# Kernel tuning notes

Measured on AMD Instinct MI355X. Metric: run time of the kernel, lower is better.

The kernel has to match this reference:

```python
import jax, jax.numpy as jnp
import numpy as np

F_TOT = 108
OUT_CH = 5
GNN_IN = 5


def setup_inputs() -> dict:
    key = jax.random.key(0)
    ks = jax.random.split(key, 24)
    B, S, N, E = 16, 1, 20000, 320000
    s = 0.1  # param init scale
    d = {}
    d["x"] = jax.random.normal(ks[0], (B, S, N, F_TOT), jnp.float32)
    d["edge_index"] = jax.random.randint(ks[1], (2, E), 0, N, dtype=jnp.int32)
    # four Conv1d(1, 5, k=24) branches
    for i, nm in enumerate(["t", "r", "tp", "ssr"]):
        d[f"w_{nm}"] = s * jax.random.normal(ks[2 + 2 * i], (OUT_CH, 1, 24), jnp.float32)
        d[f"b_{nm}"] = s * jax.random.normal(ks[3 + 2 * i], (OUT_CH,), jnp.float32)
    # fc1: 32 -> 20, fc2: 20 -> 5
    d["fc1_w"] = s * jax.random.normal(ks[10], (20, 12 + 4 * OUT_CH), jnp.float32)
    d["fc1_b"] = s * jax.random.normal(ks[11], (20,), jnp.float32)
    d["fc2_w"] = s * jax.random.normal(ks[12], (GNN_IN, 20), jnp.float32)
    d["fc2_b"] = s * jax.random.normal(ks[13], (GNN_IN,), jnp.float32)
    # SAGEConv(5 -> 20): lin_l (with bias, applied to mean-aggregated neighbors), lin_r (no bias, root)
    d["g1_wl"] = s * jax.random.normal(ks[14], (20, GNN_IN), jnp.float32)
    d["g1_bl"] = s * jax.random.normal(ks[15], (20,), jnp.float32)
    d["g1_wr"] = s * jax.random.normal(ks[16], (20, GNN_IN), jnp.float32)
    # SAGEConv(20 -> 1)
    d["g2_wl"] = s * jax.random.normal(ks[17], (1, 20), jnp.float32)
    d["g2_bl"] = s * jax.random.normal(ks[18], (1,), jnp.float32)
    d["g2_wr"] = s * jax.random.normal(ks[19], (1, 20), jnp.float32)
    return d


def _branch(xs, w, b):
    # Conv1d(in=1, out=5, k=24) over a length-24 window == a single dot product per channel.
    # xs: [NB, 24], w: [5, 1, 24] -> [NB, 5], then ReLU
    return jax.nn.relu(jnp.einsum('nk,ok->no', xs, w[:, 0, :]) + b)


def _sage(h, src, dst, wl, bl, wr, n_nodes):
    # PyG SAGEConv with mean aggregation: out = lin_l(mean_{j in N(i)} x_j) + lin_r(x_i)
    # h: [B, N, d]
    msg = jnp.transpose(h[:, src, :], (1, 0, 2))                    # [E, B, d]
    agg = jax.ops.segment_sum(msg, dst, num_segments=n_nodes)       # [N, B, d]
    deg = jax.ops.segment_sum(jnp.ones((src.shape[0],), h.dtype), dst, num_segments=n_nodes)
    mean = jnp.transpose(agg, (1, 0, 2)) / jnp.maximum(deg, 1.0)[None, :, None]  # [B, N, d]
    return mean @ wl.T + bl + h @ wr.T


def reference(x, edge_index, w_t, b_t, w_r, b_r, w_tp, b_tp, w_ssr, b_ssr,
              fc1_w, fc1_b, fc2_w, fc2_b, g1_wl, g1_bl, g1_wr, g2_wl, g2_bl, g2_wr):
    B, S, N, F = x.shape
    src, dst = edge_index[0], edge_index[1]
    # permute(2,0,1,3).reshape(N*B, S, F); S == 1
    xs = jnp.transpose(x, (2, 0, 1, 3)).reshape(N * B, S, F)[:, 0, :]  # [NB, 108]
    out_t = _branch(xs[:, 12:36], w_t, b_t)
    out_r = _branch(xs[:, 36:60], w_r, b_r)
    out_tp = _branch(xs[:, 60:84], w_tp, b_tp)
    out_ssr = _branch(xs[:, 84:108], w_ssr, b_ssr)
    feat = jnp.concatenate([xs[:, :12], out_t, out_r, out_tp, out_ssr], axis=1)  # [NB, 32]
    h = jax.nn.relu(feat @ fc1_w.T + fc1_b) @ fc2_w.T + fc2_b                    # [NB, 5]
    h = jnp.transpose(h.reshape(N, B, -1), (1, 0, 2))                            # [B, N, 5]
    h = _sage(h, src, dst, g1_wl, g1_bl, g1_wr, N)                               # [B, N, 20]
    h = _sage(h, src, dst, g2_wl, g2_bl, g2_wr, N)                               # [B, N, 1]
    return jnp.transpose(h, (0, 2, 1))                                           # [B, 1, N]
```

## Files before the change

### kernel.cpp

```cpp
#include <hip/hip_runtime.h>


__global__ void k_coefs(const float* __restrict__ g1_wl, const float* __restrict__ g1_bl,
                        const float* __restrict__ g1_wr, const float* __restrict__ g2_wl,
                        const float* __restrict__ g2_wr, float* __restrict__ coef) {
  if (blockIdx.x == 0 && threadIdx.x == 0) {
    for (int k = 0; k < 5; ++k) {
      float a = 0.f, r1 = 0.f, c = 0.f, r2 = 0.f;
      for (int j = 0; j < 20; ++j) {
        float wl = g1_wl[j * 5 + k], wr = g1_wr[j * 5 + k];
        a  += g2_wl[j] * wl;
        r1 += g2_wr[j] * wl;
        c  += g2_wl[j] * wr;
        r2 += g2_wr[j] * wr;
      }
      coef[k] = a; coef[5 + k] = r1; coef[10 + k] = c; coef[15 + k] = r2;
    }
    float kb1 = 0.f, kb2 = 0.f;
    for (int j = 0; j < 20; ++j) { kb1 += g2_wl[j] * g1_bl[j]; kb2 += g2_wr[j] * g1_bl[j]; }
    coef[20] = kb1; coef[21] = kb2;
  }
}

__global__ void k_deg(const int* __restrict__ dst, int E, int* __restrict__ degi) {
  int e = blockIdx.x * blockDim.x + threadIdx.x;
  if (e < E) atomicAdd(&degi[dst[e]], 1);
}

__global__ void k_inv(const int* __restrict__ degi, float* __restrict__ invd, int N) {
  int n = blockIdx.x * blockDim.x + threadIdx.x;
  if (n < N) invd[n] = 1.0f / fmaxf((float)degi[n], 1.0f);
}

__global__ __launch_bounds__(256) void k_mlp(
    const float* __restrict__ x,
    const float* __restrict__ w_t, const float* __restrict__ b_t,
    const float* __restrict__ w_r, const float* __restrict__ b_r,
    const float* __restrict__ w_tp, const float* __restrict__ b_tp,
    const float* __restrict__ w_ssr, const float* __restrict__ b_ssr,
    const float* __restrict__ f1w, const float* __restrict__ f1b,
    const float* __restrict__ f2w, const float* __restrict__ f2b,
    const float* __restrict__ coef,
    float* __restrict__ F1, float* __restrict__ F2, int N, int rows) {
  int rr = blockIdx.x * 256 + threadIdx.x;
  if (rr >= rows) return;
  const float* xp = x + (size_t)rr * 108;

  float feat[32];
#pragma unroll
  for (int i = 0; i < 3; ++i) {
    float4 v = *reinterpret_cast<const float4*>(xp + 4 * i);
    feat[4 * i + 0] = v.x; feat[4 * i + 1] = v.y; feat[4 * i + 2] = v.z; feat[4 * i + 3] = v.w;
  }
  const float* cw[4] = {w_t, w_r, w_tp, w_ssr};
  const float* cb[4] = {b_t, b_r, b_tp, b_ssr};
#pragma unroll
  for (int br = 0; br < 4; ++br) {
    float win[24];
#pragma unroll
    for (int i = 0; i < 6; ++i) {
      float4 v = *reinterpret_cast<const float4*>(xp + 12 + br * 24 + 4 * i);
      win[4 * i + 0] = v.x; win[4 * i + 1] = v.y; win[4 * i + 2] = v.z; win[4 * i + 3] = v.w;
    }
#pragma unroll
    for (int o = 0; o < 5; ++o) {
      float acc = cb[br][o];
#pragma unroll
      for (int k = 0; k < 24; ++k) acc = fmaf(win[k], cw[br][o * 24 + k], acc);
      feat[12 + br * 5 + o] = fmaxf(acc, 0.f);
    }
  }
  float h20[20];
#pragma unroll
  for (int o = 0; o < 20; ++o) {
    float acc = f1b[o];
#pragma unroll
    for (int i = 0; i < 32; ++i) acc = fmaf(feat[i], f1w[o * 32 + i], acc);
    h20[o] = fmaxf(acc, 0.f);
  }
  float h5[5];
#pragma unroll
  for (int o = 0; o < 5; ++o) {
    float acc = f2b[o];
#pragma unroll
    for (int i = 0; i < 20; ++i) acc = fmaf(h20[i], f2w[o * 20 + i], acc);
    h5[o] = acc;
  }
  float sa = 0.f, sr1 = 0.f, sc = 0.f, sr2 = 0.f;
#pragma unroll
  for (int k = 0; k < 5; ++k) {
    sa  = fmaf(h5[k], coef[k],      sa);
    sr1 = fmaf(h5[k], coef[5 + k],  sr1);
    sc  = fmaf(h5[k], coef[10 + k], sc);
    sr2 = fmaf(h5[k], coef[15 + k], sr2);
  }
  int b = rr / N;
  int n = rr - b * N;
  reinterpret_cast<float2*>(F1)[n * 16 + b] = make_float2(sa, sr1);
  reinterpret_cast<float2*>(F2)[n * 16 + b] = make_float2(sc, sr2);
}

__global__ void k_agg1(const int* __restrict__ src, const int* __restrict__ dst, int E,
                       const float* __restrict__ F1, float* __restrict__ A1) {
  int t = blockIdx.x * blockDim.x + threadIdx.x;
  int e = t >> 5, j = t & 31;
  if (e < E) {
    int s = src[e], d = dst[e];
    atomicAdd(&A1[d * 32 + j], F1[s * 32 + j]);
  }
}

__global__ void k_fin1(const float* __restrict__ A1, const float* __restrict__ F2,
                       const float* __restrict__ invd, float* __restrict__ W, int N) {
  int t = blockIdx.x * blockDim.x + threadIdx.x;
  if (t < N * 16) {
    int n = t >> 4, b = t & 15;
    W[t] = A1[n * 32 + 2 * b] * invd[n] + F2[n * 32 + 2 * b];
  }
}

__global__ void k_agg2(const int* __restrict__ src, const int* __restrict__ dst, int E,
                       const float* __restrict__ W, float* __restrict__ A2) {
  int t = blockIdx.x * blockDim.x + threadIdx.x;
  int e = t >> 4, b = t & 15;
  if (e < E) {
    int s = src[e], d = dst[e];
    atomicAdd(&A2[d * 16 + b], W[s * 16 + b]);
  }
}

__global__ void k_final(const float* __restrict__ A1, const float* __restrict__ F2,
                        const float* __restrict__ A2, const float* __restrict__ invd,
                        const int* __restrict__ degi, const float* __restrict__ coef,
                        const float* __restrict__ g2_bl, float* __restrict__ out, int N) {
  int t = blockIdx.x * blockDim.x + threadIdx.x;
  if (t < 16 * N) {
    int b = t / N, n = t - b * N;
    float inv = invd[n];
    float chi = degi[n] > 0 ? 1.f : 0.f;
    float kb1 = coef[20], kb2 = coef[21], bl2 = g2_bl[0];
    out[t] = (A2[n * 16 + b] + A1[n * 32 + 2 * b + 1]) * inv
             + F2[n * 32 + 2 * b + 1] + kb1 * chi + kb2 + bl2;
  }
}

extern "C" void kernel_launch(void* const* d_in, const int* in_sizes, int n_in,
                              void* d_out, int out_size, void* d_ws, size_t ws_size,
                              hipStream_t stream) {
  const float* x     = (const float*)d_in[0];
  const int*   ei    = (const int*)d_in[1];
  const float* w_t   = (const float*)d_in[2];
  const float* b_t   = (const float*)d_in[3];
  const float* w_r   = (const float*)d_in[4];
  const float* b_r   = (const float*)d_in[5];
  const float* w_tp  = (const float*)d_in[6];
  const float* b_tp  = (const float*)d_in[7];
  const float* w_ssr = (const float*)d_in[8];
  const float* b_ssr = (const float*)d_in[9];
  const float* f1w   = (const float*)d_in[10];
  const float* f1b   = (const float*)d_in[11];
  const float* f2w   = (const float*)d_in[12];
  const float* f2b   = (const float*)d_in[13];
  const float* g1_wl = (const float*)d_in[14];
  const float* g1_bl = (const float*)d_in[15];
  const float* g1_wr = (const float*)d_in[16];
  const float* g2_wl = (const float*)d_in[17];
  const float* g2_bl = (const float*)d_in[18];
  const float* g2_wr = (const float*)d_in[19];
  float* out = (float*)d_out;

  const int E = in_sizes[1] / 2;
  const int N = out_size / 16;
  const int rows = out_size;
  const int* src = ei;
  const int* dst = ei + E;

  float* ws   = (float*)d_ws;
  float* coef = ws;
  int*   degi = (int*)(ws + 32);
  float* invd = ws + 32 + N;
  float* F1   = invd + N;
  float* F2   = F1 + (size_t)32 * N;
  float* A1   = F2 + (size_t)32 * N;
  float* A2   = A1 + (size_t)32 * N;
  float* W    = A2 + (size_t)16 * N;

  hipMemsetAsync(degi, 0, (size_t)N * sizeof(int), stream);
  hipMemsetAsync(A1, 0, (size_t)N * 32 * sizeof(float), stream);
  hipMemsetAsync(A2, 0, (size_t)N * 16 * sizeof(float), stream);

  k_coefs<<<1, 64, 0, stream>>>(g1_wl, g1_bl, g1_wr, g2_wl, g2_wr, coef);
  k_deg<<<(E + 255) / 256, 256, 0, stream>>>(dst, E, degi);
  k_inv<<<(N + 255) / 256, 256, 0, stream>>>(degi, invd, N);
  k_mlp<<<(rows + 255) / 256, 256, 0, stream>>>(
      x, w_t, b_t, w_r, b_r, w_tp, b_tp, w_ssr, b_ssr,
      f1w, f1b, f2w, f2b, coef, F1, F2, N, rows);
  {
    long long t1 = (long long)E * 32;
    k_agg1<<<(int)((t1 + 255) / 256), 256, 0, stream>>>(src, dst, E, F1, A1);
  }
  k_fin1<<<(N * 16 + 255) / 256, 256, 0, stream>>>(A1, F2, invd, W, N);
  {
    long long t2 = (long long)E * 16;
    k_agg2<<<(int)((t2 + 255) / 256), 256, 0, stream>>>(src, dst, E, W, A2);
  }
  k_final<<<(16 * N + 255) / 256, 256, 0, stream>>>(A1, F2, A2, invd, degi, coef, g2_bl, out, N);
}
```

Measured before the change: 149.6 us.

## Fuse memsets, degree count and coefficient precompute into existing kernels

Removes the three memsets and the coefficient, degree and inverse-degree kernels. Zeroing of the accumulators and degree array moves into the MLP kernel, and degree counting moves into the first aggregation, which now uses 16 threads per edge with float2 loads. Inverse degree and the SAGE coefficient contractions are recomputed inline in each thread, adding some arithmetic per thread. The MLP kernel also preloads the whole 108-float row into registers and reorders the conv loops. The aim is to cut kernel-launch count and extra passes over memory.

```diff
diff --git a/kernel.cpp b/kernel.cpp
--- a/kernel.cpp
+++ b/kernel.cpp
@@ -1,36 +1,5 @@
 #include <hip/hip_runtime.h>
 
-
-__global__ void k_coefs(const float* __restrict__ g1_wl, const float* __restrict__ g1_bl,
-                        const float* __restrict__ g1_wr, const float* __restrict__ g2_wl,
-                        const float* __restrict__ g2_wr, float* __restrict__ coef) {
-  if (blockIdx.x == 0 && threadIdx.x == 0) {
-    for (int k = 0; k < 5; ++k) {
-      float a = 0.f, r1 = 0.f, c = 0.f, r2 = 0.f;
-      for (int j = 0; j < 20; ++j) {
-        float wl = g1_wl[j * 5 + k], wr = g1_wr[j * 5 + k];
-        a  += g2_wl[j] * wl;
-        r1 += g2_wr[j] * wl;
-        c  += g2_wl[j] * wr;
-        r2 += g2_wr[j] * wr;
-      }
-      coef[k] = a; coef[5 + k] = r1; coef[10 + k] = c; coef[15 + k] = r2;
-    }
-    float kb1 = 0.f, kb2 = 0.f;
-    for (int j = 0; j < 20; ++j) { kb1 += g2_wl[j] * g1_bl[j]; kb2 += g2_wr[j] * g1_bl[j]; }
-    coef[20] = kb1; coef[21] = kb2;
-  }
-}
-
-__global__ void k_deg(const int* __restrict__ dst, int E, int* __restrict__ degi) {
-  int e = blockIdx.x * blockDim.x + threadIdx.x;
-  if (e < E) atomicAdd(&degi[dst[e]], 1);
-}
-
-__global__ void k_inv(const int* __restrict__ degi, float* __restrict__ invd, int N) {
-  int n = blockIdx.x * blockDim.x + threadIdx.x;
-  if (n < N) invd[n] = 1.0f / fmaxf((float)degi[n], 1.0f);
-}
 
 __global__ __launch_bounds__(256) void k_mlp(
     const float* __restrict__ x,
@@ -40,36 +9,47 @@
     const float* __restrict__ w_ssr, const float* __restrict__ b_ssr,
     const float* __restrict__ f1w, const float* __restrict__ f1b,
     const float* __restrict__ f2w, const float* __restrict__ f2b,
-    const float* __restrict__ coef,
-    float* __restrict__ F1, float* __restrict__ F2, int N, int rows) {
+    const float* __restrict__ g1_wl, const float* __restrict__ g1_wr,
+    const float* __restrict__ g2_wl, const float* __restrict__ g2_wr,
+    float* __restrict__ F1, float* __restrict__ F2,
+    int* __restrict__ degi, float* __restrict__ A1, float* __restrict__ A2,
+    int N, int rows) {
   int rr = blockIdx.x * 256 + threadIdx.x;
   if (rr >= rows) return;
-  const float* xp = x + (size_t)rr * 108;
+
+  const float4* xv = reinterpret_cast<const float4*>(x + (size_t)rr * 108);
+  float4 v[27];
+#pragma unroll
+  for (int i = 0; i < 27; ++i) v[i] = xv[i];
 
   float feat[32];
 #pragma unroll
   for (int i = 0; i < 3; ++i) {
-    float4 v = *reinterpret_cast<const float4*>(xp + 4 * i);
-    feat[4 * i + 0] = v.x; feat[4 * i + 1] = v.y; feat[4 * i + 2] = v.z; feat[4 * i + 3] = v.w;
+    feat[4 * i + 0] = v[i].x; feat[4 * i + 1] = v[i].y;
+    feat[4 * i + 2] = v[i].z; feat[4 * i + 3] = v[i].w;
   }
   const float* cw[4] = {w_t, w_r, w_tp, w_ssr};
   const float* cb[4] = {b_t, b_r, b_tp, b_ssr};
 #pragma unroll
   for (int br = 0; br < 4; ++br) {
-    float win[24];
+    float acc[5];
 #pragma unroll
-    for (int i = 0; i < 6; ++i) {
-      float4 v = *reinterpret_cast<const float4*>(xp + 12 + br * 24 + 4 * i);
-      win[4 * i + 0] = v.x; win[4 * i + 1] = v.y; win[4 * i + 2] = v.z; win[4 * i + 3] = v.w;
+    for (int o = 0; o < 5; ++o) acc[o] = cb[br][o];
+#pragma unroll
+    for (int q = 0; q < 6; ++q) {
+      float4 w4 = v[3 + 6 * br + q];
+#pragma unroll
+      for (int o = 0; o < 5; ++o) {
+        acc[o] = fmaf(w4.x, cw[br][o * 24 + 4 * q + 0], acc[o]);
+        acc[o] = fmaf(w4.y, cw[br][o * 24 + 4 * q + 1], acc[o]);
+        acc[o] = fmaf(w4.z, cw[br][o * 24 + 4 * q + 2], acc[o]);
+        acc[o] = fmaf(w4.w, cw[br][o * 24 + 4 * q + 3], acc[o]);
+      }
     }
 #pragma unroll
-    for (int o = 0; o < 5; ++o) {
-      float acc = cb[br][o];
-#pragma unroll
-      for (int k = 0; k < 24; ++k) acc = fmaf(win[k], cw[br][o * 24 + k], acc);
-      feat[12 + br * 5 + o] = fmaxf(acc, 0.f);
-    }
+    for (int o = 0; o < 5; ++o) feat[12 + br * 5 + o] = fmaxf(acc[o], 0.f);
   }
+
   float h20[20];
 #pragma unroll
   for (int o = 0; o < 20; ++o) {
@@ -86,36 +66,52 @@
     for (int i = 0; i < 20; ++i) acc = fmaf(h20[i], f2w[o * 20 + i], acc);
     h5[o] = acc;
   }
+
   float sa = 0.f, sr1 = 0.f, sc = 0.f, sr2 = 0.f;
 #pragma unroll
-  for (int k = 0; k < 5; ++k) {
-    sa  = fmaf(h5[k], coef[k],      sa);
-    sr1 = fmaf(h5[k], coef[5 + k],  sr1);
-    sc  = fmaf(h5[k], coef[10 + k], sc);
-    sr2 = fmaf(h5[k], coef[15 + k], sr2);
+  for (int j = 0; j < 20; ++j) {
+    float t1 = 0.f, t2 = 0.f;
+#pragma unroll
+    for (int k = 0; k < 5; ++k) {
+      t1 = fmaf(g1_wl[j * 5 + k], h5[k], t1);
+      t2 = fmaf(g1_wr[j * 5 + k], h5[k], t2);
+    }
+    float wl2 = g2_wl[j], wr2 = g2_wr[j];
+    sa  = fmaf(wl2, t1, sa);
+    sr1 = fmaf(wr2, t1, sr1);
+    sc  = fmaf(wl2, t2, sc);
+    sr2 = fmaf(wr2, t2, sr2);
   }
+
   int b = rr / N;
   int n = rr - b * N;
   reinterpret_cast<float2*>(F1)[n * 16 + b] = make_float2(sa, sr1);
   reinterpret_cast<float2*>(F2)[n * 16 + b] = make_float2(sc, sr2);
+  reinterpret_cast<float2*>(A1)[n * 16 + b] = make_float2(0.f, 0.f);
+  A2[n * 16 + b] = 0.f;
+  if (b == 0) degi[n] = 0;
 }
 
 __global__ void k_agg1(const int* __restrict__ src, const int* __restrict__ dst, int E,
-                       const float* __restrict__ F1, float* __restrict__ A1) {
+                       const float* __restrict__ F1, float* __restrict__ A1,
+                       int* __restrict__ degi) {
   int t = blockIdx.x * blockDim.x + threadIdx.x;
-  int e = t >> 5, j = t & 31;
-  if (e < E) {
-    int s = src[e], d = dst[e];
-    atomicAdd(&A1[d * 32 + j], F1[s * 32 + j]);
-  }
+  int e = t >> 4, b = t & 15;
+  if (e >= E) return;
+  int s = src[e], d = dst[e];
+  float2 f = reinterpret_cast<const float2*>(F1)[s * 16 + b];
+  atomicAdd(&A1[d * 32 + 2 * b + 0], f.x);
+  atomicAdd(&A1[d * 32 + 2 * b + 1], f.y);
+  if (b == 0) atomicAdd(&degi[d], 1);
 }
 
 __global__ void k_fin1(const float* __restrict__ A1, const float* __restrict__ F2,
-                       const float* __restrict__ invd, float* __restrict__ W, int N) {
+                       const int* __restrict__ degi, float* __restrict__ W, int N) {
   int t = blockIdx.x * blockDim.x + threadIdx.x;
   if (t < N * 16) {
     int n = t >> 4, b = t & 15;
-    W[t] = A1[n * 32 + 2 * b] * invd[n] + F2[n * 32 + 2 * b];
+    float inv = 1.0f / fmaxf((float)degi[n], 1.0f);
+    W[t] = A1[n * 32 + 2 * b] * inv + F2[n * 32 + 2 * b];
   }
 }
 
@@ -123,24 +119,29 @@
                        const float* __restrict__ W, float* __restrict__ A2) {
   int t = blockIdx.x * blockDim.x + threadIdx.x;
   int e = t >> 4, b = t & 15;
-  if (e < E) {
-    int s = src[e], d = dst[e];
-    atomicAdd(&A2[d * 16 + b], W[s * 16 + b]);
-  }
+  if (e >= E) return;
+  int s = src[e], d = dst[e];
+  atomicAdd(&A2[d * 16 + b], W[s * 16 + b]);
 }
 
 __global__ void k_final(const float* __restrict__ A1, const float* __restrict__ F2,
-                        const float* __restrict__ A2, const float* __restrict__ invd,
-                        const int* __restrict__ degi, const float* __restrict__ coef,
-                        const float* __restrict__ g2_bl, float* __restrict__ out, int N) {
+                        const float* __restrict__ A2, const int* __restrict__ degi,
+                        const float* __restrict__ g1_bl, const float* __restrict__ g2_wl,
+                        const float* __restrict__ g2_wr, const float* __restrict__ g2_bl,
+                        float* __restrict__ out, int N) {
   int t = blockIdx.x * blockDim.x + threadIdx.x;
   if (t < 16 * N) {
     int b = t / N, n = t - b * N;
-    float inv = invd[n];
+    float kb1 = 0.f, kb2 = 0.f;
+#pragma unroll
+    for (int j = 0; j < 20; ++j) {
+      kb1 = fmaf(g2_wl[j], g1_bl[j], kb1);
+      kb2 = fmaf(g2_wr[j], g1_bl[j], kb2);
+    }
+    float inv = 1.0f / fmaxf((float)degi[n], 1.0f);
     float chi = degi[n] > 0 ? 1.f : 0.f;
-    float kb1 = coef[20], kb2 = coef[21], bl2 = g2_bl[0];
     out[t] = (A2[n * 16 + b] + A1[n * 32 + 2 * b + 1]) * inv
-             + F2[n * 32 + 2 * b + 1] + kb1 * chi + kb2 + bl2;
+             + F2[n * 32 + 2 * b + 1] + kb1 * chi + kb2 + g2_bl[0];
   }
 }
 
@@ -175,34 +176,23 @@
   const int* src = ei;
   const int* dst = ei + E;
 
-  float* ws   = (float*)d_ws;
-  float* coef = ws;
-  int*   degi = (int*)(ws + 32);
-  float* invd = ws + 32 + N;
-  float* F1   = invd + N;
-  float* F2   = F1 + (size_t)32 * N;
-  float* A1   = F2 + (size_t)32 * N;
-  float* A2   = A1 + (size_t)32 * N;
-  float* W    = A2 + (size_t)16 * N;
+  float* ws = (float*)d_ws;
+  float* F1 = ws;
+  float* F2 = F1 + (size_t)32 * N;
+  float* A1 = F2 + (size_t)32 * N;
+  float* A2 = A1 + (size_t)32 * N;
+  float* W  = A2 + (size_t)16 * N;
+  int* degi = (int*)(W + (size_t)16 * N);
 
-  hipMemsetAsync(degi, 0, (size_t)N * sizeof(int), stream);
-  hipMemsetAsync(A1, 0, (size_t)N * 32 * sizeof(float), stream);
-  hipMemsetAsync(A2, 0, (size_t)N * 16 * sizeof(float), stream);
-
-  k_coefs<<<1, 64, 0, stream>>>(g1_wl, g1_bl, g1_wr, g2_wl, g2_wr, coef);
-  k_deg<<<(E + 255) / 256, 256, 0, stream>>>(dst, E, degi);
-  k_inv<<<(N + 255) / 256, 256, 0, stream>>>(degi, invd, N);
   k_mlp<<<(rows + 255) / 256, 256, 0, stream>>>(
       x, w_t, b_t, w_r, b_r, w_tp, b_tp, w_ssr, b_ssr,
-      f1w, f1b, f2w, f2b, coef, F1, F2, N, rows);
-  {
-    long long t1 = (long long)E * 32;
-    k_agg1<<<(int)((t1 + 255) / 256), 256, 0, stream>>>(src, dst, E, F1, A1);
-  }
-  k_fin1<<<(N * 16 + 255) / 256, 256, 0, stream>>>(A1, F2, invd, W, N);
-  {
-    long long t2 = (long long)E * 16;
-    k_agg2<<<(int)((t2 + 255) / 256), 256, 0, stream>>>(src, dst, E, W, A2);
-  }
-  k_final<<<(16 * N + 255) / 256, 256, 0, stream>>>(A1, F2, A2, invd, degi, coef, g2_bl, out, N);
+      f1w, f1b, f2w, f2b, g1_wl, g1_wr, g2_wl, g2_wr,
+      F1, F2, degi, A1, A2, N, rows);
+
+  int tE = ((E * 16) + 255) / 256;
+  k_agg1<<<tE, 256, 0, stream>>>(src, dst, E, F1, A1, degi);
+  k_fin1<<<(N * 16 + 255) / 256, 256, 0, stream>>>(A1, F2, degi, W, N);
+  k_agg2<<<tE, 256, 0, stream>>>(src, dst, E, W, A2);
+  k_final<<<(N * 16 + 255) / 256, 256, 0, stream>>>(
+      A1, F2, A2, degi, g1_bl, g2_wl, g2_wr, g2_bl, out, N);
 }
```

Result: slower. 165.3 us (+10.5%).
